# Optimization experiments

Hardware: AMD Instinct MI355X
Metric: run time of the kernel (lower is better)

Reference implementation:

```python
import jax, jax.numpy as jnp
import numpy as np

D_MODEL = 2048
NUM_HEADS = 16
HEAD_DIM = D_MODEL // NUM_HEADS
BATCH = 2
SEQ = 2048


def setup_inputs() -> dict:
    key = jax.random.key(0)
    ks = jax.random.split(key, 5)
    s = 1.0 / np.sqrt(D_MODEL)
    return {
        "x": jax.random.normal(ks[0], (BATCH, SEQ, D_MODEL), dtype=jnp.float32),
        "Wq": jax.random.normal(ks[1], (D_MODEL, D_MODEL), dtype=jnp.float32) * s,
        "Wk": jax.random.normal(ks[2], (D_MODEL, D_MODEL), dtype=jnp.float32) * s,
        "Wv": jax.random.normal(ks[3], (D_MODEL, D_MODEL), dtype=jnp.float32) * s,
        "Wo": jax.random.normal(ks[4], (D_MODEL, D_MODEL), dtype=jnp.float32) * s,
    }


def reference(x, Wq, Wk, Wv, Wo):
    B, S, D = x.shape
    H, Dh = NUM_HEADS, HEAD_DIM
    # nn.Linear(bias=False): y = x @ W.T ; split_heads is a plain view (no transpose!)
    Q = (x @ Wq.T).reshape(B, H, S, Dh)
    K = (x @ Wk.T).reshape(B, H, S, Dh)
    V = (x @ Wv.T).reshape(B, H, S, Dh)
    # scores scaled by head_dim (NOT sqrt) — faithful to source
    scores = jnp.einsum("bhqd,bhkd->bhqk", Q, K) / jnp.float32(Dh)
    causal_mask = jnp.triu(jnp.ones((S, S), dtype=bool), k=1)  # True above diagonal
    scores = jnp.where(causal_mask, -jnp.inf, scores)
    attn = jax.nn.softmax(scores, axis=-1)
    out = jnp.einsum("bhqk,bhkd->bhqd", attn, V)  # [B,H,S,Dh]
    out = out.transpose(0, 2, 1, 3).reshape(B, S, D)  # merge DOES transpose
    return out @ Wo.T
```

## Files before the change

### kernel.cpp

```cpp
#include <hip/hip_runtime.h>
#include <hip/hip_bf16.h>

using bf16 = __hip_bfloat16;
typedef __attribute__((ext_vector_type(8))) short bf16x8;
typedef __attribute__((ext_vector_type(4))) float f32x4;

#define DEVI __device__ __forceinline__

constexpr int Bn = 2, Sn = 2048, Dn = 2048, Hn = 16, DHn = 128;
constexpr int Mn = Bn * Sn;

DEVI void gload_lds16(const bf16* g, bf16* l) {
  __builtin_amdgcn_global_load_lds(
      (__attribute__((address_space(1))) void*)g,
      (__attribute__((address_space(3))) void*)l,
      16, 0, 0);
}

__global__ __launch_bounds__(256) void cvt_bf16_k(const float* __restrict__ in,
                                                  bf16* __restrict__ out, int n8) {
  int i = blockIdx.x * 256 + threadIdx.x;
  if (i >= n8) return;
  const float4* p = (const float4*)in + (size_t)i * 2;
  float4 a = p[0], b = p[1];
  union { bf16 h[8]; bf16x8 v; } u;
  u.h[0] = __float2bfloat16(a.x); u.h[1] = __float2bfloat16(a.y);
  u.h[2] = __float2bfloat16(a.z); u.h[3] = __float2bfloat16(a.w);
  u.h[4] = __float2bfloat16(b.x); u.h[5] = __float2bfloat16(b.y);
  u.h[6] = __float2bfloat16(b.z); u.h[7] = __float2bfloat16(b.w);
  *((bf16x8*)out + i) = u.v;
}

template <int OUTF32, int NTOT, int NMAT, int MW>
__global__ __launch_bounds__(256, 2) void gemmZ(const bf16* __restrict__ A,
                                                const bf16* __restrict__ W,
                                                void* __restrict__ Cv) {
  constexpr int K = 2048, NT = K / 32;
  constexpr int BM = MW * 32;
  constexpr int SLOT = (BM + 128) * 32;
  __shared__ bf16 smem[2 * SLOT];

  constexpr int MT = Mn / BM;
  const int nwg = NTOT * MT;
  const int orig = blockIdx.x;
  const int wgid = (orig & 7) * (nwg >> 3) + (orig >> 3);
  const int bm = wgid / NTOT;
  const int bnn = wgid % NTOT;
  constexpr int nper = NTOT / NMAT;
  const int z = bnn / nper;
  const int col0 = (bnn % nper) * 128;

  const int t = threadIdx.x;
  const int wave = t >> 6, lane = t & 63;
  const int wm = wave >> 1, wn = wave & 1;
  const int lr = lane & 15, lg = lane >> 4;
  const int rch = ((lg ^ ((lr >> 1) & 3)) * 8);
  const int srow = t >> 2;
  const int sch = (t & 3) ^ ((t >> 3) & 3);

  const bf16* Ab = A + (size_t)(bm * BM + srow) * K + sch * 8;
  const bf16* Bb = W + (size_t)z * (2048 * 2048) +
                   (size_t)(col0 + srow) * K + sch * 8;

  auto stgA = [&](int slot, int kt, int u) {
    gload_lds16(Ab + (size_t)u * 64 * K + kt * 32,
                smem + slot * SLOT + u * 2048 + t * 8);
  };
  auto stgB = [&](int slot, int kt, int v) {
    gload_lds16(Bb + (size_t)v * 64 * K + kt * 32,
                smem + slot * SLOT + BM * 32 + v * 2048 + t * 8);
  };

  f32x4 acc[MW][4];
  const f32x4 zf = {0.f, 0.f, 0.f, 0.f};
#pragma unroll
  for (int i = 0; i < MW; ++i)
#pragma unroll
    for (int j = 0; j < 4; ++j) acc[i][j] = zf;

#pragma unroll
  for (int u = 0; u < MW / 2; ++u) stgA(0, 0, u);
  stgB(0, 0, 0); stgB(0, 0, 1);

#pragma unroll 2
  for (int kt = 0; kt < NT; ++kt) {
    const int slot = kt & 1;
    const bf16* sAb = smem + slot * SLOT;
    const bf16* sBb = sAb + BM * 32;

    asm volatile("s_waitcnt vmcnt(0)" ::: "memory");
    __builtin_amdgcn_sched_barrier(0);
    __builtin_amdgcn_s_barrier();
    __builtin_amdgcn_sched_barrier(0);

    if (kt + 1 < NT) {
#pragma unroll
      for (int u = 0; u < MW / 2; ++u) stgA(slot ^ 1, kt + 1, u);
      stgB(slot ^ 1, kt + 1, 0); stgB(slot ^ 1, kt + 1, 1);
    }

    bf16x8 bv[4], af[MW];
#pragma unroll
    for (int n = 0; n < 4; ++n)
      bv[n] = *(const bf16x8*)(sBb + (wn * 64 + n * 16 + lr) * 32 + rch);
#pragma unroll
    for (int i = 0; i < MW; ++i)
      af[i] = *(const bf16x8*)(sAb + (wm * (MW * 16) + i * 16 + lr) * 32 + rch);

    __builtin_amdgcn_s_setprio(1);
#pragma unroll
    for (int i = 0; i < MW; ++i)
#pragma unroll
      for (int n = 0; n < 4; ++n)
        acc[i][n] = __builtin_amdgcn_mfma_f32_16x16x32_bf16(af[i], bv[n], acc[i][n], 0, 0, 0);
    __builtin_amdgcn_s_setprio(0);
    __builtin_amdgcn_sched_barrier(0);
  }

  const int r0 = bm * BM + wm * (MW * 16), c0 = col0 + wn * 64;
#pragma unroll
  for (int mm = 0; mm < MW; ++mm)
#pragma unroll
    for (int nn = 0; nn < 4; ++nn) {
      const int rr = r0 + mm * 16 + lg * 4;
      const int cc = c0 + nn * 16 + lr;
#pragma unroll
      for (int r = 0; r < 4; ++r) {
        float v = acc[mm][nn][r];
        if (OUTF32) {
          ((float*)Cv)[(size_t)(rr + r) * 2048 + cc] = v;
        } else {
          bf16* C = (bf16*)Cv + (size_t)z * (Mn * 2048);
          C[(size_t)(rr + r) * 2048 + cc] = __float2bfloat16(v);
        }
      }
    }
}

__global__ __launch_bounds__(256, 2) void transpose_v(const bf16* __restrict__ V,
                                                      bf16* __restrict__ VT) {
  __shared__ bf16 tile[128 * 128];
  const int kt = blockIdx.x, bh = blockIdx.y;
  const bf16* Vh = V + (size_t)bh * (Sn * DHn);
  bf16* VTh = VT + (size_t)bh * (DHn * Sn);
  const int t = threadIdx.x;
  const int rr = t >> 4, cc = t & 15;
#pragma unroll
  for (int i = 0; i < 8; ++i) {
    int r = rr + i * 16;
    int ch = cc ^ ((r >> 3) & 7);
    *(bf16x8*)(tile + r * 128 + ch * 8) =
        *(const bf16x8*)(Vh + (size_t)(kt * 128 + r) * DHn + cc * 8);
  }
  __syncthreads();
  const int dr = t >> 4, li = t & 15;
#pragma unroll
  for (int i = 0; i < 8; ++i) {
    int dh = dr + i * 16;
    union { bf16 h[8]; bf16x8 v; } u;
#pragma unroll
    for (int j = 0; j < 8; ++j) {
      int k = li * 8 + j;
      int ch = (dh >> 3) ^ ((k >> 3) & 7);
      u.h[j] = tile[k * 128 + ch * 8 + (dh & 7)];
    }
    *(bf16x8*)(VTh + (size_t)dh * Sn + kt * 128 + li * 8) = u.v;
  }
}

__global__ __launch_bounds__(512, 1) void attn_k3(const bf16* __restrict__ Q,
                                                  const bf16* __restrict__ K,
                                                  const bf16* __restrict__ VT,
                                                  bf16* __restrict__ Mg) {
  __shared__ bf16 smem[40960];
  bf16* sK0 = smem;
  bf16* sK1 = smem + 8192;
  bf16* sV0 = smem + 16384;
  bf16* sV1 = smem + 24576;
  bf16* sP  = smem + 32768;
  bf16* sO  = smem;

  const int j = blockIdx.x;
  const int bh = blockIdx.y;
  const bf16* Qh = Q + (size_t)bh * (Sn * DHn);
  const bf16* Kh = K + (size_t)bh * (Sn * DHn);
  const bf16* VTh = VT + (size_t)bh * (DHn * Sn);
  const int b = bh >> 4, h = bh & 15;

  const int t = threadIdx.x, wave = t >> 6, lane = t & 63;
  const int lr = lane & 15, lg = lane >> 4;

  auto STAGE = [&](int buf, int kt) {
    bf16* dK = buf ? sK1 : sK0;
    bf16* dV = buf ? sV1 : sV0;
#pragma unroll
    for (int i = 0; i < 2; ++i) {
      int c = i * 512 + t;
      int row = c >> 4, c16 = c & 15;
      gload_lds16(Kh + (size_t)(kt * 64 + row) * DHn + ((c16 ^ (row & 7)) * 8),
                  dK + c * 8);
    }
#pragma unroll
    for (int i = 0; i < 2; ++i) {
      int c = i * 512 + t;
      int row = c >> 3, c8 = c & 7;
      gload_lds16(VTh + (size_t)row * Sn + kt * 64 + ((c8 ^ (row & 7)) * 8),
                  dV + c * 8);
    }
  };

  const f32x4 zf = {0.f, 0.f, 0.f, 0.f};

  for (int pi = 0; pi < 2; ++pi) {
    const int qb = pi ? (15 - j) : j;
    const int nt = qb * 2 + 2;
    const int q0 = qb * 128 + wave * 16;

    bf16x8 qf[4];
#pragma unroll
    for (int kk = 0; kk < 4; ++kk)
      qf[kk] = *(const bf16x8*)(Qh + (size_t)(q0 + lr) * DHn + kk * 32 + lg * 8);

    f32x4 o[8];
#pragma unroll
    for (int d = 0; d < 8; ++d) o[d] = zf;
    float mrun[4], lrun[4];
#pragma unroll
    for (int r = 0; r < 4; ++r) { mrun[r] = -3e38f; lrun[r] = 0.f; }

    STAGE(0, 0);
    __syncthreads();
    int cur = 0;

    for (int kt = 0; kt < nt; ++kt) {
      if (kt + 1 < nt) STAGE(cur ^ 1, kt + 1);

      bf16* sKc = cur ? sK1 : sK0;
      bf16* sVc = cur ? sV1 : sV0;

      f32x4 sfr[4];
#pragma unroll
      for (int nn = 0; nn < 4; ++nn) sfr[nn] = zf;
#pragma unroll
      for (int kk = 0; kk < 4; ++kk)
#pragma unroll
        for (int nn = 0; nn < 4; ++nn) {
          int row = nn * 16 + lr;
          int ch = (kk * 4 + lg) ^ (row & 7);
          bf16x8 kf = *(const bf16x8*)(sKc + row * DHn + ch * 8);
          sfr[nn] = __builtin_amdgcn_mfma_f32_16x16x32_bf16(qf[kk], kf, sfr[nn], 0, 0, 0);
        }

      const bool maskt = (kt >= qb * 2);
      float pv[4][4];
#pragma unroll
      for (int nn = 0; nn < 4; ++nn)
#pragma unroll
        for (int r = 0; r < 4; ++r) {
          float v = sfr[nn][r] * (1.0f / 128.0f);
          if (maskt) {
            int kg = kt * 64 + nn * 16 + lr;
            int qg = q0 + lg * 4 + r;
            if (kg > qg) v = -1e30f;
          }
          pv[nn][r] = v;
        }
      float mnew[4], alpha[4], rsum[4];
#pragma unroll
      for (int r = 0; r < 4; ++r) {
        float rm = fmaxf(fmaxf(pv[0][r], pv[1][r]), fmaxf(pv[2][r], pv[3][r]));
        rm = fmaxf(rm, __shfl_xor(rm, 1));
        rm = fmaxf(rm, __shfl_xor(rm, 2));
        rm = fmaxf(rm, __shfl_xor(rm, 4));
        rm = fmaxf(rm, __shfl_xor(rm, 8));
        mnew[r] = fmaxf(mrun[r], rm);
        alpha[r] = __expf(mrun[r] - mnew[r]);
        mrun[r] = mnew[r];
        rsum[r] = 0.f;
      }
#pragma unroll
      for (int nn = 0; nn < 4; ++nn)
#pragma unroll
        for (int r = 0; r < 4; ++r) {
          float p = __expf(pv[nn][r] - mnew[r]);
          pv[nn][r] = p;
          rsum[r] += p;
        }
#pragma unroll
      for (int r = 0; r < 4; ++r) {
        float s = rsum[r];
        s += __shfl_xor(s, 1); s += __shfl_xor(s, 2);
        s += __shfl_xor(s, 4); s += __shfl_xor(s, 8);
        lrun[r] = lrun[r] * alpha[r] + s;
      }
#pragma unroll
      for (int d = 0; d < 8; ++d)
#pragma unroll
        for (int r = 0; r < 4; ++r) o[d][r] *= alpha[r];

#pragma unroll
      for (int nn = 0; nn < 4; ++nn)
#pragma unroll
        for (int r = 0; r < 4; ++r) {
          int row = lg * 4 + r;
          int chk = (nn * 2 + (lr >> 3)) ^ (row & 7);
          sP[wave * 1024 + row * 64 + chk * 8 + (lr & 7)] = __float2bfloat16(pv[nn][r]);
        }

      bf16x8 pf[2];
#pragma unroll
      for (int kk = 0; kk < 2; ++kk) {
        int ch = (kk * 4 + lg) ^ (lr & 7);
        pf[kk] = *(const bf16x8*)(sP + wave * 1024 + lr * 64 + ch * 8);
      }
#pragma unroll
      for (int d = 0; d < 8; ++d)
#pragma unroll
        for (int kk = 0; kk < 2; ++kk) {
          int vrow = d * 16 + lr;
          int vch = (kk * 4 + lg) ^ (vrow & 7);
          bf16x8 vf = *(const bf16x8*)(sVc + vrow * 64 + vch * 8);
          o[d] = __builtin_amdgcn_mfma_f32_16x16x32_bf16(pf[kk], vf, o[d], 0, 0, 0);
        }

      __syncthreads();
      cur ^= 1;
    }

    float inv[4];
#pragma unroll
    for (int r = 0; r < 4; ++r) inv[r] = 1.0f / lrun[r];
#pragma unroll
    for (int d = 0; d < 8; ++d)
#pragma unroll
      for (int r = 0; r < 4; ++r) {
        int row = wave * 16 + lg * 4 + r;
        int col = d * 16 + lr;
        int chk = ((col >> 3) ^ (row & 7));
        sO[row * 128 + chk * 8 + (col & 7)] = __float2bfloat16(o[d][r] * inv[r]);
      }
    __syncthreads();
    bf16* Mh = Mg + ((size_t)(b * Sn + qb * 128)) * Dn + h * DHn;
#pragma unroll
    for (int i = 0; i < 4; ++i) {
      int row = (t >> 4) + i * 32;
      int c16 = t & 15;
      *(bf16x8*)(Mh + (size_t)row * Dn + c16 * 8) =
          *(const bf16x8*)(sO + row * 128 + ((c16 ^ (row & 7)) * 8));
    }
    __syncthreads();
  }
}

extern "C" void kernel_launch(void* const* d_in, const int* in_sizes, int n_in,
                              void* d_out, int out_size, void* d_ws, size_t ws_size,
                              hipStream_t stream) {
  const float* x = (const float*)d_in[0];
  const float* Wq = (const float*)d_in[1];
  const float* Wk = (const float*)d_in[2];
  const float* Wv = (const float*)d_in[3];
  const float* Wo = (const float*)d_in[4];
  float* out = (float*)d_out;

  char* ws = (char*)d_ws;
  bf16* xb = (bf16*)ws;            ws += (size_t)Mn * Dn * 2;
  bf16* Wb = (bf16*)ws;            ws += (size_t)4 * Dn * Dn * 2;
  bf16* QKV = (bf16*)ws;           ws += (size_t)3 * Mn * Dn * 2;
  bf16* VT = (bf16*)ws;            ws += (size_t)Bn * Hn * DHn * Sn * 2;
  bf16* Mg = (bf16*)ws;            ws += (size_t)Mn * Dn * 2;

  const int nx8 = Mn * Dn / 8;
  const int nw8 = Dn * Dn / 8;
  cvt_bf16_k<<<nx8 / 256, 256, 0, stream>>>(x, xb, nx8);
  cvt_bf16_k<<<nw8 / 256, 256, 0, stream>>>(Wq, Wb + 0 * (size_t)Dn * Dn, nw8);
  cvt_bf16_k<<<nw8 / 256, 256, 0, stream>>>(Wk, Wb + 1 * (size_t)Dn * Dn, nw8);
  cvt_bf16_k<<<nw8 / 256, 256, 0, stream>>>(Wv, Wb + 2 * (size_t)Dn * Dn, nw8);
  cvt_bf16_k<<<nw8 / 256, 256, 0, stream>>>(Wo, Wb + 3 * (size_t)Dn * Dn, nw8);

  gemmZ<0, 48, 3, 8><<<768, 256, 0, stream>>>(xb, Wb, (void*)QKV);

  transpose_v<<<dim3(16, 32), 256, 0, stream>>>(QKV + 2 * (size_t)Mn * Dn, VT);

  attn_k3<<<dim3(8, 32), 512, 0, stream>>>(QKV, QKV + (size_t)Mn * Dn, VT, Mg);

  gemmZ<1, 16, 1, 4><<<512, 256, 0, stream>>>(Mg, Wb + 3 * (size_t)Dn * Dn, (void*)out);
}
```

Baseline: 268.7 us.

## Use triple-buffered LDS pipeline in GEMMs and fuse conversion kernels

Measured after the change: 258.5 us. -3.8%, faster.

```diff
diff --git a/kernel.cpp b/kernel.cpp
--- a/kernel.cpp
+++ b/kernel.cpp
@@ -17,28 +17,43 @@
       16, 0, 0);
 }
 
-__global__ __launch_bounds__(256) void cvt_bf16_k(const float* __restrict__ in,
-                                                  bf16* __restrict__ out, int n8) {
-  int i = blockIdx.x * 256 + threadIdx.x;
-  if (i >= n8) return;
-  const float4* p = (const float4*)in + (size_t)i * 2;
-  float4 a = p[0], b = p[1];
-  union { bf16 h[8]; bf16x8 v; } u;
-  u.h[0] = __float2bfloat16(a.x); u.h[1] = __float2bfloat16(a.y);
-  u.h[2] = __float2bfloat16(a.z); u.h[3] = __float2bfloat16(a.w);
-  u.h[4] = __float2bfloat16(b.x); u.h[5] = __float2bfloat16(b.y);
-  u.h[6] = __float2bfloat16(b.z); u.h[7] = __float2bfloat16(b.w);
-  *((bf16x8*)out + i) = u.v;
+__global__ __launch_bounds__(256) void cvt_all_k(const float* __restrict__ x,
+                                                 const float* __restrict__ wq,
+                                                 const float* __restrict__ wk,
+                                                 const float* __restrict__ wv,
+                                                 const float* __restrict__ wo,
+                                                 bf16* __restrict__ xb,
+                                                 bf16* __restrict__ wb) {
+  const int which = blockIdx.y;
+  const float* src;
+  bf16* dst;
+  int n8;
+  if (which == 0) { src = x;  dst = xb; n8 = Mn * Dn / 8; }
+  else {
+    src = (which == 1) ? wq : (which == 2) ? wk : (which == 3) ? wv : wo;
+    dst = wb + (size_t)(which - 1) * Dn * Dn;
+    n8 = Dn * Dn / 8;
+  }
+  for (int i = blockIdx.x * 256 + threadIdx.x; i < n8; i += gridDim.x * 256) {
+    const float4* p = (const float4*)src + (size_t)i * 2;
+    float4 a = p[0], b = p[1];
+    union { bf16 h[8]; bf16x8 v; } u;
+    u.h[0] = __float2bfloat16(a.x); u.h[1] = __float2bfloat16(a.y);
+    u.h[2] = __float2bfloat16(a.z); u.h[3] = __float2bfloat16(a.w);
+    u.h[4] = __float2bfloat16(b.x); u.h[5] = __float2bfloat16(b.y);
+    u.h[6] = __float2bfloat16(b.z); u.h[7] = __float2bfloat16(b.w);
+    *((bf16x8*)dst + i) = u.v;
+  }
 }
 
 template <int OUTF32, int NTOT, int NMAT, int MW>
-__global__ __launch_bounds__(256, 2) void gemmZ(const bf16* __restrict__ A,
-                                                const bf16* __restrict__ W,
-                                                void* __restrict__ Cv) {
+__global__ __launch_bounds__(256, 2) void gemm3s(const bf16* __restrict__ A,
+                                                 const bf16* __restrict__ W,
+                                                 void* __restrict__ Cv) {
   constexpr int K = 2048, NT = K / 32;
   constexpr int BM = MW * 32;
   constexpr int SLOT = (BM + 128) * 32;
-  __shared__ bf16 smem[2 * SLOT];
+  __shared__ bf16 smem[3 * SLOT];
 
   constexpr int MT = Mn / BM;
   const int nwg = NTOT * MT;
@@ -70,6 +85,11 @@
     gload_lds16(Bb + (size_t)v * 64 * K + kt * 32,
                 smem + slot * SLOT + BM * 32 + v * 2048 + t * 8);
   };
+  auto stage_tile = [&](int slot, int kt) {
+#pragma unroll
+    for (int u = 0; u < MW / 2; ++u) stgA(slot, kt, u);
+    stgB(slot, kt, 0); stgB(slot, kt, 1);
+  };
 
   f32x4 acc[MW][4];
   const f32x4 zf = {0.f, 0.f, 0.f, 0.f};
@@ -78,25 +98,23 @@
 #pragma unroll
     for (int j = 0; j < 4; ++j) acc[i][j] = zf;
 
-#pragma unroll
-  for (int u = 0; u < MW / 2; ++u) stgA(0, 0, u);
-  stgB(0, 0, 0); stgB(0, 0, 1);
-
-#pragma unroll 2
+  stage_tile(0, 0);
+  stage_tile(1, 1);
+
+  int slot = 0;
+#pragma unroll 1
   for (int kt = 0; kt < NT; ++kt) {
-    const int slot = kt & 1;
     const bf16* sAb = smem + slot * SLOT;
     const bf16* sBb = sAb + BM * 32;
 
-    asm volatile("s_waitcnt vmcnt(0)" ::: "memory");
-    __builtin_amdgcn_sched_barrier(0);
+    if (kt == NT - 1)            asm volatile("s_waitcnt vmcnt(0)" ::: "memory");
+    else if constexpr (MW == 8)  asm volatile("s_waitcnt vmcnt(6)" ::: "memory");
+    else                         asm volatile("s_waitcnt vmcnt(4)" ::: "memory");
     __builtin_amdgcn_s_barrier();
-    __builtin_amdgcn_sched_barrier(0);
-
-    if (kt + 1 < NT) {
-#pragma unroll
-      for (int u = 0; u < MW / 2; ++u) stgA(slot ^ 1, kt + 1, u);
-      stgB(slot ^ 1, kt + 1, 0); stgB(slot ^ 1, kt + 1, 1);
+
+    if (kt + 2 < NT) {
+      int ps = slot + 2; if (ps >= 3) ps -= 3;
+      stage_tile(ps, kt + 2);
     }
 
     bf16x8 bv[4], af[MW];
@@ -114,7 +132,8 @@
       for (int n = 0; n < 4; ++n)
         acc[i][n] = __builtin_amdgcn_mfma_f32_16x16x32_bf16(af[i], bv[n], acc[i][n], 0, 0, 0);
     __builtin_amdgcn_s_setprio(0);
-    __builtin_amdgcn_sched_barrier(0);
+
+    slot = (slot == 2) ? 0 : slot + 1;
   }
 
   const int r0 = bm * BM + wm * (MW * 16), c0 = col0 + wn * 64;
@@ -369,19 +388,13 @@
   bf16* VT = (bf16*)ws;            ws += (size_t)Bn * Hn * DHn * Sn * 2;
   bf16* Mg = (bf16*)ws;            ws += (size_t)Mn * Dn * 2;
 
-  const int nx8 = Mn * Dn / 8;
-  const int nw8 = Dn * Dn / 8;
-  cvt_bf16_k<<<nx8 / 256, 256, 0, stream>>>(x, xb, nx8);
-  cvt_bf16_k<<<nw8 / 256, 256, 0, stream>>>(Wq, Wb + 0 * (size_t)Dn * Dn, nw8);
-  cvt_bf16_k<<<nw8 / 256, 256, 0, stream>>>(Wk, Wb + 1 * (size_t)Dn * Dn, nw8);
-  cvt_bf16_k<<<nw8 / 256, 256, 0, stream>>>(Wv, Wb + 2 * (size_t)Dn * Dn, nw8);
-  cvt_bf16_k<<<nw8 / 256, 256, 0, stream>>>(Wo, Wb + 3 * (size_t)Dn * Dn, nw8);
-
-  gemmZ<0, 48, 3, 8><<<768, 256, 0, stream>>>(xb, Wb, (void*)QKV);
+  cvt_all_k<<<dim3(2048, 5), 256, 0, stream>>>(x, Wq, Wk, Wv, Wo, xb, Wb);
+
+  gemm3s<0, 48, 3, 8><<<768, 256, 0, stream>>>(xb, Wb, (void*)QKV);
 
   transpose_v<<<dim3(16, 32), 256, 0, stream>>>(QKV + 2 * (size_t)Mn * Dn, VT);
 
   attn_k3<<<dim3(8, 32), 512, 0, stream>>>(QKV, QKV + (size_t)Mn * Dn, VT, Mg);
 
-  gemmZ<1, 16, 1, 4><<<512, 256, 0, stream>>>(Mg, Wb + 3 * (size_t)Dn * Dn, (void*)out);
-}
+  gemm3s<1, 16, 1, 4><<<512, 256, 0, stream>>>(Mg, Wb + 3 * (size_t)Dn * Dn, (void*)out);
+}
```
